# Kernel tuning notes

Measured on AMD Instinct MI355X. Metric: run time of the kernel, lower is better.

The kernel has to match this reference:

```python
import jax, jax.numpy as jnp
import numpy as np

SCALING = 32.0 / 16.0  # alpha / r

def setup_inputs() -> dict:
    key = jax.random.key(0)
    k1, k2, k3, k4 = jax.random.split(key, 4)
    B_, S, D_in, D_out, R = 4, 2048, 4096, 4096, 16
    x = jax.random.normal(k1, (B_, S, D_in), dtype=jnp.float32)
    W_base = jax.random.normal(k2, (D_out, D_in), dtype=jnp.float32) * 0.02
    b_base = jax.random.normal(k3, (D_out,), dtype=jnp.float32) * 0.02
    A = jax.random.normal(k4, (R, D_in), dtype=jnp.float32) * 0.02
    B = jnp.zeros((D_out, R), dtype=jnp.float32)  # lora_B init to zeros
    return {"x": x, "W_base": W_base, "b_base": b_base, "A": A, "B": B}

def reference(x, W_base, b_base, A, B):
    # base linear (stands in for dequantized 4-bit matmul): [B,S,Din] @ [Din,Dout]
    out = jnp.einsum('bsd,od->bso', x, W_base) + b_base
    # LoRA path: B(A(x)) * scaling, dropout=0 -> identity
    xa = jnp.einsum('bsd,rd->bsr', x, A)        # [B,S,r]
    delta = jnp.einsum('bsr,or->bso', xa, B)    # [B,S,Dout]
    return out + delta * SCALING
```

## Files before the change

### kernel.cpp

```cpp
#include <hip/hip_runtime.h>


typedef __attribute__((ext_vector_type(4))) float f32x4;
typedef __attribute__((ext_vector_type(8))) short bf16x8;

__device__ __forceinline__ unsigned short f2bf(float f) {
    unsigned u = __builtin_bit_cast(unsigned, f);
    unsigned r = u + 0x7fffu + ((u >> 16) & 1u);
    return (unsigned short)(r >> 16);
}

__device__ __forceinline__ void gload_lds16(const void* g, void* l) {
    __builtin_amdgcn_global_load_lds(
        (const __attribute__((address_space(1))) void*)g,
        (__attribute__((address_space(3))) void*)l, 16, 0, 0);
}

__global__ __launch_bounds__(256) void cast_x_kernel(
    const float* __restrict__ x, unsigned short* __restrict__ xb, int n8)
{
    int stride = gridDim.x * blockDim.x;
    for (int i = blockIdx.x * blockDim.x + threadIdx.x; i < n8; i += stride) {
        size_t base = (size_t)i * 8;
        float4 f0 = *(const float4*)&x[base];
        float4 f1 = *(const float4*)&x[base + 4];
        ushort4 o0, o1;
        o0.x = f2bf(f0.x); o0.y = f2bf(f0.y); o0.z = f2bf(f0.z); o0.w = f2bf(f0.w);
        o1.x = f2bf(f1.x); o1.y = f2bf(f1.y); o1.z = f2bf(f1.z); o1.w = f2bf(f1.w);
        *(ushort4*)&xb[base]     = o0;
        *(ushort4*)&xb[base + 4] = o1;
    }
}

__global__ __launch_bounds__(256) void prep_w_kernel(
    const float* __restrict__ W, const float* __restrict__ A,
    const float* __restrict__ Bl, unsigned short* __restrict__ wb,
    int K, float scale)
{
    __shared__ float Bs[16][16];
    const int t = threadIdx.x;
    const int n0 = blockIdx.y * 16;
    const int k0 = blockIdx.x * 256;
    {
        int nl = t >> 4, r = t & 15;
        Bs[nl][r] = Bl[(size_t)(n0 + nl) * 16 + r];
    }
    __syncthreads();

    const int lane = t & 63;
    const int wv = t >> 6;
    const int k = k0 + lane * 4;

    float4 av[16];
#pragma unroll
    for (int r = 0; r < 16; ++r)
        av[r] = *(const float4*)&A[(size_t)r * K + k];

#pragma unroll
    for (int j = 0; j < 4; ++j) {
        const int nl = wv * 4 + j;
        const int n = n0 + nl;
        float4 w = *(const float4*)&W[(size_t)n * K + k];
        float d0 = 0.f, d1 = 0.f, d2 = 0.f, d3 = 0.f;
#pragma unroll
        for (int r = 0; r < 16; ++r) {
            float b = Bs[nl][r];
            d0 += b * av[r].x; d1 += b * av[r].y;
            d2 += b * av[r].z; d3 += b * av[r].w;
        }
        ushort4 o;
        o.x = f2bf(w.x + scale * d0);
        o.y = f2bf(w.y + scale * d1);
        o.z = f2bf(w.z + scale * d2);
        o.w = f2bf(w.w + scale * d3);
        *(ushort4*)&wb[(size_t)n * K + k] = o;
    }
}


#define SETPRIO(p) __builtin_amdgcn_s_setprio(p)
#define BARRIER()  __builtin_amdgcn_s_barrier()

__global__ __launch_bounds__(512, 2) void gemm256_kernel(
    const unsigned short* __restrict__ Xb, const unsigned short* __restrict__ Wb,
    const float* __restrict__ bias, float* __restrict__ out,
    int M, int N, int K)
{
    __shared__ __align__(16) unsigned short lds[2][2][2][8192];

    const int NT = K / 64;
    const int ntn = N / 256;
    int bid = blockIdx.x;
    {
        int per = gridDim.x >> 3;
        bid = (bid & 7) * per + (bid >> 3);
    }
    const int tm = bid / ntn, tn = bid % ntn;

    const int t = threadIdx.x;
    const int lane = t & 63, wave = t >> 6;
    const int wr = wave >> 2;
    const int wc = wave & 3;

    const int srow = t >> 3;
    const int scol = ((t & 7) * 8) ^ (((t >> 3) & 7) << 3);
    unsigned gA[2][2], gB[2][2];
#pragma unroll
    for (int h = 0; h < 2; ++h)
#pragma unroll
        for (int i = 0; i < 2; ++i) {
            gA[h][i] = (unsigned)((tm * 256 + h * 128 + i * 64 + srow) * K + scol);
            gB[h][i] = (unsigned)((tn * 256 + h * 128 + i * 64 + srow) * K + scol);
        }

#define STAGE_A(buf, kt)                                                        \
    _Pragma("unroll") for (int h = 0; h < 2; ++h)                               \
    _Pragma("unroll") for (int i = 0; i < 2; ++i)                               \
        gload_lds16(Xb + gA[h][i] + (kt) * 64,                                  \
                    &lds[buf][0][h][i * 4096 + wave * 512]);
#define STAGE_B(buf, kt)                                                        \
    _Pragma("unroll") for (int h = 0; h < 2; ++h)                               \
    _Pragma("unroll") for (int i = 0; i < 2; ++i)                               \
        gload_lds16(Wb + gB[h][i] + (kt) * 64,                                  \
                    &lds[buf][1][h][i * 4096 + wave * 512]);

    const int fr = lane & 15;
    const int hi16 = ((lane >> 4) & 3) * 16;
    const int bsw = (fr & 7) << 4;
    const int lo0 = hi16 ^ bsw;
    const int lo1 = (64 + hi16) ^ bsw;

    f32x4 acc[8][4] = {};
    bf16x8 a[8][2], b[4][2];

    STAGE_A(0, 0); STAGE_B(0, 0);
    STAGE_A(1, 1); STAGE_B(1, 1);
    asm volatile("s_waitcnt vmcnt(8)" ::: "memory");
    BARRIER();

    for (int kt = 0; kt < NT; ++kt) {
        const int cur = kt & 1;
        const char* pA = (const char*)&lds[cur][0][wr][0];
        const char* pB = (const char*)&lds[cur][1][wc >> 1][0];
        const int bro = (wc & 1) * 64;

#pragma unroll
        for (int mi = 0; mi < 4; ++mi) {
            a[mi][0] = *(const bf16x8*)(pA + (mi * 16 + fr) * 128 + lo0);
            a[mi][1] = *(const bf16x8*)(pA + (mi * 16 + fr) * 128 + lo1);
        }
#pragma unroll
        for (int ni = 0; ni < 2; ++ni) {
            b[ni][0] = *(const bf16x8*)(pB + (bro + ni * 16 + fr) * 128 + lo0);
            b[ni][1] = *(const bf16x8*)(pB + (bro + ni * 16 + fr) * 128 + lo1);
        }
        BARRIER();
        SETPRIO(1);
#pragma unroll
        for (int mi = 0; mi < 4; ++mi)
#pragma unroll
            for (int ni = 0; ni < 2; ++ni)
#pragma unroll
                for (int kk = 0; kk < 2; ++kk)
                    acc[mi][ni] = __builtin_amdgcn_mfma_f32_16x16x32_bf16(
                        a[mi][kk], b[ni][kk], acc[mi][ni], 0, 0, 0);
        SETPRIO(0);
        BARRIER();

#pragma unroll
        for (int mi = 4; mi < 8; ++mi) {
            a[mi][0] = *(const bf16x8*)(pA + (mi * 16 + fr) * 128 + lo0);
            a[mi][1] = *(const bf16x8*)(pA + (mi * 16 + fr) * 128 + lo1);
        }
#pragma unroll
        for (int ni = 2; ni < 4; ++ni) {
            b[ni][0] = *(const bf16x8*)(pB + (bro + ni * 16 + fr) * 128 + lo0);
            b[ni][1] = *(const bf16x8*)(pB + (bro + ni * 16 + fr) * 128 + lo1);
        }
        BARRIER();
        SETPRIO(1);
#pragma unroll
        for (int mi = 0; mi < 4; ++mi)
#pragma unroll
            for (int ni = 2; ni < 4; ++ni)
#pragma unroll
                for (int kk = 0; kk < 2; ++kk)
                    acc[mi][ni] = __builtin_amdgcn_mfma_f32_16x16x32_bf16(
                        a[mi][kk], b[ni][kk], acc[mi][ni], 0, 0, 0);
        SETPRIO(0);
        asm volatile("s_waitcnt lgkmcnt(0)" ::: "memory");
        BARRIER();

        if (kt + 2 < NT) { STAGE_A(cur, kt + 2); }
        BARRIER();
        SETPRIO(1);
#pragma unroll
        for (int mi = 4; mi < 8; ++mi)
#pragma unroll
            for (int ni = 0; ni < 2; ++ni)
#pragma unroll
                for (int kk = 0; kk < 2; ++kk)
                    acc[mi][ni] = __builtin_amdgcn_mfma_f32_16x16x32_bf16(
                        a[mi][kk], b[ni][kk], acc[mi][ni], 0, 0, 0);
        SETPRIO(0);
        BARRIER();

        if (kt + 2 < NT) {
            STAGE_B(cur, kt + 2);
            asm volatile("s_waitcnt vmcnt(8)" ::: "memory");
        } else {
            asm volatile("s_waitcnt vmcnt(0)" ::: "memory");
        }
        BARRIER();
        SETPRIO(1);
#pragma unroll
        for (int mi = 4; mi < 8; ++mi)
#pragma unroll
            for (int ni = 2; ni < 4; ++ni)
#pragma unroll
                for (int kk = 0; kk < 2; ++kk)
                    acc[mi][ni] = __builtin_amdgcn_mfma_f32_16x16x32_bf16(
                        a[mi][kk], b[ni][kk], acc[mi][ni], 0, 0, 0);
        SETPRIO(0);
        BARRIER();
    }

    const int row0 = tm * 256 + wr * 128 + (lane >> 4) * 4;
    const int col0 = tn * 256 + wc * 64;
#pragma unroll
    for (int ni = 0; ni < 4; ++ni) {
        const int col = col0 + ni * 16 + fr;
        const float bv = bias[col];
#pragma unroll
        for (int mi = 0; mi < 8; ++mi) {
            const int row = row0 + mi * 16;
#pragma unroll
            for (int r = 0; r < 4; ++r)
                out[(size_t)(row + r) * N + col] = acc[mi][ni][r] + bv;
        }
    }
}

extern "C" void kernel_launch(void* const* d_in, const int* in_sizes, int n_in,
                              void* d_out, int out_size, void* d_ws, size_t ws_size,
                              hipStream_t stream)
{
    const float* x  = (const float*)d_in[0];
    const float* W  = (const float*)d_in[1];
    const float* b  = (const float*)d_in[2];
    const float* A  = (const float*)d_in[3];
    const float* Bl = (const float*)d_in[4];
    float* out = (float*)d_out;

    const int Dout = in_sizes[2];
    const int Din  = in_sizes[1] / Dout;
    const int M    = in_sizes[0] / Din;

    unsigned short* xb = (unsigned short*)d_ws;
    unsigned short* wb = xb + (size_t)M * Din;

    cast_x_kernel<<<2048, 256, 0, stream>>>(x, xb, M * Din / 8);

    dim3 gw(Din / 256, Dout / 16);
    prep_w_kernel<<<gw, 256, 0, stream>>>(W, A, Bl, wb, Din, 2.0f);

    const int grid = (M / 256) * (Dout / 256);
    gemm256_kernel<<<grid, 512, 0, stream>>>(xb, wb, b, out, M, Dout, Din);
}
```

Baseline: 323.1 us.

## Replace four-phase ping-pong schedule with single load-all then compute-all iteration

Removes the interleaved four-quadrant MFMA schedule, which used s_setprio and many barriers to overlap LDS reads and global-to-LDS staging with compute. Each k-step now loads all A and B fragments from LDS, runs all 64 MFMAs, waits for LDS, then issues both A and B prefetches together. This cuts barrier and priority overhead but loses fine-grained overlap between waves, and it holds all fragments live at once, which raises register pressure under the 2-blocks-per-CU launch bound.

```diff
diff --git a/kernel.cpp b/kernel.cpp
--- a/kernel.cpp
+++ b/kernel.cpp
@@ -78,7 +78,6 @@
 }
 
 
-#define SETPRIO(p) __builtin_amdgcn_s_setprio(p)
 #define BARRIER()  __builtin_amdgcn_s_barrier()
 
 __global__ __launch_bounds__(512, 2) void gemm256_kernel(
@@ -131,7 +130,6 @@
     const int lo1 = (64 + hi16) ^ bsw;
 
     f32x4 acc[8][4] = {};
-    bf16x8 a[8][2], b[4][2];
 
     STAGE_A(0, 0); STAGE_B(0, 0);
     STAGE_A(1, 1); STAGE_B(1, 1);
@@ -144,84 +142,35 @@
         const char* pB = (const char*)&lds[cur][1][wc >> 1][0];
         const int bro = (wc & 1) * 64;
 
-#pragma unroll
-        for (int mi = 0; mi < 4; ++mi) {
+        bf16x8 a[8][2], b[4][2];
+#pragma unroll
+        for (int mi = 0; mi < 8; ++mi) {
             a[mi][0] = *(const bf16x8*)(pA + (mi * 16 + fr) * 128 + lo0);
             a[mi][1] = *(const bf16x8*)(pA + (mi * 16 + fr) * 128 + lo1);
         }
 #pragma unroll
-        for (int ni = 0; ni < 2; ++ni) {
+        for (int ni = 0; ni < 4; ++ni) {
             b[ni][0] = *(const bf16x8*)(pB + (bro + ni * 16 + fr) * 128 + lo0);
             b[ni][1] = *(const bf16x8*)(pB + (bro + ni * 16 + fr) * 128 + lo1);
         }
-        BARRIER();
-        SETPRIO(1);
-#pragma unroll
-        for (int mi = 0; mi < 4; ++mi)
-#pragma unroll
-            for (int ni = 0; ni < 2; ++ni)
-#pragma unroll
-                for (int kk = 0; kk < 2; ++kk)
+
+#pragma unroll
+        for (int kk = 0; kk < 2; ++kk)
+#pragma unroll
+            for (int mi = 0; mi < 8; ++mi)
+#pragma unroll
+                for (int ni = 0; ni < 4; ++ni)
                     acc[mi][ni] = __builtin_amdgcn_mfma_f32_16x16x32_bf16(
                         a[mi][kk], b[ni][kk], acc[mi][ni], 0, 0, 0);
-        SETPRIO(0);
-        BARRIER();
-
-#pragma unroll
-        for (int mi = 4; mi < 8; ++mi) {
-            a[mi][0] = *(const bf16x8*)(pA + (mi * 16 + fr) * 128 + lo0);
-            a[mi][1] = *(const bf16x8*)(pA + (mi * 16 + fr) * 128 + lo1);
-        }
-#pragma unroll
-        for (int ni = 2; ni < 4; ++ni) {
-            b[ni][0] = *(const bf16x8*)(pB + (bro + ni * 16 + fr) * 128 + lo0);
-            b[ni][1] = *(const bf16x8*)(pB + (bro + ni * 16 + fr) * 128 + lo1);
-        }
-        BARRIER();
-        SETPRIO(1);
-#pragma unroll
-        for (int mi = 0; mi < 4; ++mi)
-#pragma unroll
-            for (int ni = 2; ni < 4; ++ni)
-#pragma unroll
-                for (int kk = 0; kk < 2; ++kk)
-                    acc[mi][ni] = __builtin_amdgcn_mfma_f32_16x16x32_bf16(
-                        a[mi][kk], b[ni][kk], acc[mi][ni], 0, 0, 0);
-        SETPRIO(0);
+
         asm volatile("s_waitcnt lgkmcnt(0)" ::: "memory");
         BARRIER();
-
-        if (kt + 2 < NT) { STAGE_A(cur, kt + 2); }
-        BARRIER();
-        SETPRIO(1);
-#pragma unroll
-        for (int mi = 4; mi < 8; ++mi)
-#pragma unroll
-            for (int ni = 0; ni < 2; ++ni)
-#pragma unroll
-                for (int kk = 0; kk < 2; ++kk)
-                    acc[mi][ni] = __builtin_amdgcn_mfma_f32_16x16x32_bf16(
-                        a[mi][kk], b[ni][kk], acc[mi][ni], 0, 0, 0);
-        SETPRIO(0);
-        BARRIER();
-
         if (kt + 2 < NT) {
-            STAGE_B(cur, kt + 2);
+            STAGE_A(cur, kt + 2); STAGE_B(cur, kt + 2);
             asm volatile("s_waitcnt vmcnt(8)" ::: "memory");
         } else {
             asm volatile("s_waitcnt vmcnt(0)" ::: "memory");
         }
-        BARRIER();
-        SETPRIO(1);
-#pragma unroll
-        for (int mi = 4; mi < 8; ++mi)
-#pragma unroll
-            for (int ni = 2; ni < 4; ++ni)
-#pragma unroll
-                for (int kk = 0; kk < 2; ++kk)
-                    acc[mi][ni] = __builtin_amdgcn_mfma_f32_16x16x32_bf16(
-                        a[mi][kk], b[ni][kk], acc[mi][ni], 0, 0, 0);
-        SETPRIO(0);
         BARRIER();
     }
 
```

New measurement: 322.3 us. Within noise of the previous version (-0.3%).

## Interleave A/B global-to-LDS staging in quarters across MFMA phases

Applied to the files above, without the earlier changes.

Restructures the main GEMM loop so the next tile's loads are issued in small chunks between the four MFMA quarter-phases. B for tile kt+1 goes into the other buffer early in the iteration and A for kt+2 goes into the current buffer late, replacing the previous bulk A/B staging after the third and fourth phases. Explicit lgkmcnt waits with sched_barrier are added before each MFMA group, and the fragment arrays become loop-local. The aim is to spread memory traffic more evenly across compute and tighten the prologue, at the cost of more fragile wait-count and buffer-reuse correctness.

```diff
diff --git a/kernel.cpp b/kernel.cpp
--- a/kernel.cpp
+++ b/kernel.cpp
@@ -80,6 +80,8 @@
 
 #define SETPRIO(p) __builtin_amdgcn_s_setprio(p)
 #define BARRIER()  __builtin_amdgcn_s_barrier()
+#define LGKM0()    do { asm volatile("s_waitcnt lgkmcnt(0)" ::: "memory"); \
+                        __builtin_amdgcn_sched_barrier(0); } while (0)
 
 __global__ __launch_bounds__(512, 2) void gemm256_kernel(
     const unsigned short* __restrict__ Xb, const unsigned short* __restrict__ Wb,
@@ -113,16 +115,12 @@
             gB[h][i] = (unsigned)((tn * 256 + h * 128 + i * 64 + srow) * K + scol);
         }
 
-#define STAGE_A(buf, kt)                                                        \
-    _Pragma("unroll") for (int h = 0; h < 2; ++h)                               \
-    _Pragma("unroll") for (int i = 0; i < 2; ++i)                               \
-        gload_lds16(Xb + gA[h][i] + (kt) * 64,                                  \
-                    &lds[buf][0][h][i * 4096 + wave * 512]);
-#define STAGE_B(buf, kt)                                                        \
-    _Pragma("unroll") for (int h = 0; h < 2; ++h)                               \
-    _Pragma("unroll") for (int i = 0; i < 2; ++i)                               \
-        gload_lds16(Wb + gB[h][i] + (kt) * 64,                                  \
-                    &lds[buf][1][h][i * 4096 + wave * 512]);
+#define ST_A(buf, h, i, kt)                                                     \
+    gload_lds16(Xb + gA[h][i] + (kt) * 64,                                      \
+                &lds[buf][0][h][(i) * 4096 + wave * 512]);
+#define ST_B(buf, h, i, kt)                                                     \
+    gload_lds16(Wb + gB[h][i] + (kt) * 64,                                      \
+                &lds[buf][1][h][(i) * 4096 + wave * 512]);
 
     const int fr = lane & 15;
     const int hi16 = ((lane >> 4) & 3) * 16;
@@ -131,18 +129,34 @@
     const int lo1 = (64 + hi16) ^ bsw;
 
     f32x4 acc[8][4] = {};
-    bf16x8 a[8][2], b[4][2];
-
-    STAGE_A(0, 0); STAGE_B(0, 0);
-    STAGE_A(1, 1); STAGE_B(1, 1);
-    asm volatile("s_waitcnt vmcnt(8)" ::: "memory");
+
+#pragma unroll
+    for (int h = 0; h < 2; ++h)
+#pragma unroll
+        for (int i = 0; i < 2; ++i) { ST_A(0, h, i, 0) ST_B(0, h, i, 0) }
+#pragma unroll
+    for (int h = 0; h < 2; ++h)
+#pragma unroll
+        for (int i = 0; i < 2; ++i) { ST_A(1, h, i, 1) }
+    asm volatile("s_waitcnt vmcnt(4)" ::: "memory");
     BARRIER();
+
+#define MFMA_Q(m0, n0)                                                          \
+    _Pragma("unroll") for (int mi = m0; mi < m0 + 4; ++mi)                      \
+    _Pragma("unroll") for (int ni = n0; ni < n0 + 2; ++ni)                      \
+    _Pragma("unroll") for (int kk = 0; kk < 2; ++kk)                            \
+        acc[mi][ni] = __builtin_amdgcn_mfma_f32_16x16x32_bf16(                  \
+            a[mi][kk], b[ni][kk], acc[mi][ni], 0, 0, 0);
 
     for (int kt = 0; kt < NT; ++kt) {
         const int cur = kt & 1;
         const char* pA = (const char*)&lds[cur][0][wr][0];
         const char* pB = (const char*)&lds[cur][1][wc >> 1][0];
         const int bro = (wc & 1) * 64;
+        const bool stB = (kt + 1 < NT);
+        const bool stA = (kt + 2 < NT);
+
+        bf16x8 a[8][2], b[4][2];
 
 #pragma unroll
         for (int mi = 0; mi < 4; ++mi) {
@@ -154,16 +168,11 @@
             b[ni][0] = *(const bf16x8*)(pB + (bro + ni * 16 + fr) * 128 + lo0);
             b[ni][1] = *(const bf16x8*)(pB + (bro + ni * 16 + fr) * 128 + lo1);
         }
-        BARRIER();
-        SETPRIO(1);
-#pragma unroll
-        for (int mi = 0; mi < 4; ++mi)
-#pragma unroll
-            for (int ni = 0; ni < 2; ++ni)
-#pragma unroll
-                for (int kk = 0; kk < 2; ++kk)
-                    acc[mi][ni] = __builtin_amdgcn_mfma_f32_16x16x32_bf16(
-                        a[mi][kk], b[ni][kk], acc[mi][ni], 0, 0, 0);
+        if (stB) { ST_B(cur ^ 1, 0, 0, kt + 1) ST_B(cur ^ 1, 0, 1, kt + 1) }
+        BARRIER();
+        LGKM0();
+        SETPRIO(1);
+        MFMA_Q(0, 0)
         SETPRIO(0);
         BARRIER();
 
@@ -172,56 +181,37 @@
             a[mi][0] = *(const bf16x8*)(pA + (mi * 16 + fr) * 128 + lo0);
             a[mi][1] = *(const bf16x8*)(pA + (mi * 16 + fr) * 128 + lo1);
         }
+        if (stB) { ST_B(cur ^ 1, 1, 0, kt + 1) ST_B(cur ^ 1, 1, 1, kt + 1) }
+        BARRIER();
+        LGKM0();
+        SETPRIO(1);
+        MFMA_Q(4, 0)
+        SETPRIO(0);
+        BARRIER();
+
 #pragma unroll
         for (int ni = 2; ni < 4; ++ni) {
             b[ni][0] = *(const bf16x8*)(pB + (bro + ni * 16 + fr) * 128 + lo0);
             b[ni][1] = *(const bf16x8*)(pB + (bro + ni * 16 + fr) * 128 + lo1);
         }
-        BARRIER();
-        SETPRIO(1);
-#pragma unroll
-        for (int mi = 0; mi < 4; ++mi)
-#pragma unroll
-            for (int ni = 2; ni < 4; ++ni)
-#pragma unroll
-                for (int kk = 0; kk < 2; ++kk)
-                    acc[mi][ni] = __builtin_amdgcn_mfma_f32_16x16x32_bf16(
-                        a[mi][kk], b[ni][kk], acc[mi][ni], 0, 0, 0);
-        SETPRIO(0);
-        asm volatile("s_waitcnt lgkmcnt(0)" ::: "memory");
-        BARRIER();
-
-        if (kt + 2 < NT) { STAGE_A(cur, kt + 2); }
-        BARRIER();
-        SETPRIO(1);
-#pragma unroll
-        for (int mi = 4; mi < 8; ++mi)
-#pragma unroll
-            for (int ni = 0; ni < 2; ++ni)
-#pragma unroll
-                for (int kk = 0; kk < 2; ++kk)
-                    acc[mi][ni] = __builtin_amdgcn_mfma_f32_16x16x32_bf16(
-                        a[mi][kk], b[ni][kk], acc[mi][ni], 0, 0, 0);
-        SETPRIO(0);
-        BARRIER();
-
-        if (kt + 2 < NT) {
-            STAGE_B(cur, kt + 2);
-            asm volatile("s_waitcnt vmcnt(8)" ::: "memory");
+        if (stA) { ST_A(cur, 0, 0, kt + 2) ST_A(cur, 0, 1, kt + 2) }
+        BARRIER();
+        LGKM0();
+        SETPRIO(1);
+        MFMA_Q(0, 2)
+        SETPRIO(0);
+        BARRIER();
+
+        if (stA) { ST_A(cur, 1, 0, kt + 2) ST_A(cur, 1, 1, kt + 2) }
+        BARRIER();
+        SETPRIO(1);
+        MFMA_Q(4, 2)
+        SETPRIO(0);
+        if (stA) {
+            asm volatile("s_waitcnt vmcnt(4)" ::: "memory");
         } else {
             asm volatile("s_waitcnt vmcnt(0)" ::: "memory");
         }
-        BARRIER();
-        SETPRIO(1);
-#pragma unroll
-        for (int mi = 4; mi < 8; ++mi)
-#pragma unroll
-            for (int ni = 2; ni < 4; ++ni)
-#pragma unroll
-                for (int kk = 0; kk < 2; ++kk)
-                    acc[mi][ni] = __builtin_amdgcn_mfma_f32_16x16x32_bf16(
-                        a[mi][kk], b[ni][kk], acc[mi][ni], 0, 0, 0);
-        SETPRIO(0);
         BARRIER();
     }
 
```

Result: faster. 306.5 us (-5.1%).
